# Performance work log

Measured on AMD Instinct MI355X. Metric: run time of the kernel, lower is better.

Reference implementation:

```python
import jax, jax.numpy as jnp
import numpy as np

EPS = 1e-7
N_IN, N_OUT, D_IN, D_OUT = 512, 10, 8, 16  # 32*4*4 primary caps, 10 digit caps


def squash(x):
    # sum over last axis (size 1 here after the transposes, matching torch code)
    square = jnp.sum(x ** 2, axis=-1, keepdims=True)
    norm = x / (jnp.sqrt(square + EPS) + EPS)
    return (square / (1.0 + square)) * norm


def setup_inputs():
    key = jax.random.key(0)
    k1, k2 = jax.random.split(key)
    x = jax.random.normal(k1, (N_IN, D_IN), dtype=jnp.float32)
    W = jax.random.normal(k2, (1, N_IN, N_OUT, D_OUT, D_IN), dtype=jnp.float32)
    return {"x": x, "W": W}


def reference(x, W):
    # x.view(1, 512, 8, 1), then stack 10 copies along dim=2 -> (1,512,10,8,1)
    x = x.reshape(1, N_IN, D_IN, 1)
    x = jnp.broadcast_to(x[:, :, None], (1, N_IN, N_OUT, D_IN, 1))
    out1 = jnp.matmul(W, x)  # (1,512,10,16,1)  prediction vectors u_hat
    # NOTE (faithful to source): the torch loop calls softmax(self.bij) where
    # self.bij stays zeros forever (only the local `bij` is updated), and
    # nn.Softmax() with no dim on a 4D tensor softmaxes over dim=1. Hence
    # cij == 1/512 on every one of the 3 iterations, all iterations produce
    # the identical vij, and the bij/aij updates are dead code. We therefore
    # compute the (identical) final vij once.
    cij = jnp.full((1, N_IN, N_OUT, 1, 1), 1.0 / N_IN, dtype=out1.dtype)
    sij = jnp.matmul(cij, jnp.swapaxes(out1, 3, 4))  # (1,512,10,1,16)
    sij = jnp.sum(sij, axis=1, keepdims=True)        # (1,1,10,1,16)
    sij = jnp.swapaxes(sij, 3, 4)                    # (1,1,10,16,1)
    vij = squash(sij)                                # (1,1,10,16,1)
    return vij
```

## Files before the change

kernel.cpp:

```cpp
#include <hip/hip_runtime.h>


#define N_IN  512
#define N_OUT 10
#define D_OUT 16
#define D_IN  8

__global__ __launch_bounds__(256) void digitcaps_kernel(
    const float* __restrict__ x,
    const float* __restrict__ W,
    float* __restrict__ out)
{
    const int od = blockIdx.x;
    const int o  = od >> 4;
    const int d  = od & 15;
    const int t  = threadIdx.x;

    float acc = 0.0f;

    #pragma unroll
    for (int rep = 0; rep < 2; ++rep) {
        const int n = t + rep * 256;
        const float4* wp = reinterpret_cast<const float4*>(
            W + ((size_t)(n * N_OUT + o) * D_OUT + d) * D_IN);
        const float4* xp = reinterpret_cast<const float4*>(x + (size_t)n * D_IN);
        const float4 w0 = wp[0], w1 = wp[1];
        const float4 x0 = xp[0], x1 = xp[1];
        acc += w0.x * x0.x + w0.y * x0.y + w0.z * x0.z + w0.w * x0.w
             + w1.x * x1.x + w1.y * x1.y + w1.z * x1.z + w1.w * x1.w;
    }

    #pragma unroll
    for (int off = 32; off > 0; off >>= 1)
        acc += __shfl_down(acc, off, 64);

    __shared__ float wsum[4];
    const int wave = t >> 6;
    const int lane = t & 63;
    if (lane == 0) wsum[wave] = acc;
    __syncthreads();

    if (t == 0) {
        const float s    = (wsum[0] + wsum[1] + wsum[2] + wsum[3]) * (1.0f / (float)N_IN);
        const float sq   = s * s;
        const float norm = s / (sqrtf(sq + 1e-7f) + 1e-7f);
        out[od] = (sq / (1.0f + sq)) * norm;
    }
}

extern "C" void kernel_launch(void* const* d_in, const int* in_sizes, int n_in,
                              void* d_out, int out_size, void* d_ws, size_t ws_size,
                              hipStream_t stream) {
    const float* x = (const float*)d_in[0];
    const float* W = (const float*)d_in[1];
    float* out = (float*)d_out;
    digitcaps_kernel<<<dim3(N_OUT * D_OUT), dim3(256), 0, stream>>>(x, W, out);
}
```

Baseline: 57.90 us.

## Assign four adjacent output dims per block for contiguous W loads

Each block now handles one output capsule and a group of four adjacent output dimensions. Lanes are interleaved so that groups of four consecutive threads read contiguous 128-byte W segments, where before each thread read a 32-byte chunk separated by a 640-byte stride. The grid shrinks from 160 blocks to 40, each looping 8 times instead of 2, and the reduction uses xor shuffles that keep the four dimension lanes apart. The aim is better coalescing and cache-line use on the W stream. The cost is fewer blocks to spread across the GPU's compute units, which may hurt latency hiding.

```diff
diff --git a/kernel.cpp b/kernel.cpp
--- a/kernel.cpp
+++ b/kernel.cpp
@@ -11,16 +11,19 @@
     const float* __restrict__ W,
     float* __restrict__ out)
 {
-    const int od = blockIdx.x;
-    const int o  = od >> 4;
-    const int d  = od & 15;
+    const int b  = blockIdx.x;
+    const int o  = b >> 2;
+    const int dg = b & 3;
     const int t  = threadIdx.x;
+    const int dl = t & 3;
+    const int d  = dg * 4 + dl;
+    const int nb = t >> 2;
 
     float acc = 0.0f;
 
     #pragma unroll
-    for (int rep = 0; rep < 2; ++rep) {
-        const int n = t + rep * 256;
+    for (int i = 0; i < 8; ++i) {
+        const int n = nb + 64 * i;
         const float4* wp = reinterpret_cast<const float4*>(
             W + ((size_t)(n * N_OUT + o) * D_OUT + d) * D_IN);
         const float4* xp = reinterpret_cast<const float4*>(x + (size_t)n * D_IN);
@@ -31,20 +34,21 @@
     }
 
     #pragma unroll
-    for (int off = 32; off > 0; off >>= 1)
-        acc += __shfl_down(acc, off, 64);
+    for (int m = 4; m <= 32; m <<= 1)
+        acc += __shfl_xor(acc, m, 64);
 
-    __shared__ float wsum[4];
+    __shared__ float wsum[4 * 4];
     const int wave = t >> 6;
     const int lane = t & 63;
-    if (lane == 0) wsum[wave] = acc;
+    if (lane < 4) wsum[wave * 4 + lane] = acc;
     __syncthreads();
 
-    if (t == 0) {
-        const float s    = (wsum[0] + wsum[1] + wsum[2] + wsum[3]) * (1.0f / (float)N_IN);
+    if (t < 4) {
+        const float s    = (wsum[0 + t] + wsum[4 + t] + wsum[8 + t] + wsum[12 + t])
+                           * (1.0f / (float)N_IN);
         const float sq   = s * s;
         const float norm = s / (sqrtf(sq + 1e-7f) + 1e-7f);
-        out[od] = (sq / (1.0f + sq)) * norm;
+        out[o * D_OUT + dg * 4 + t] = (sq / (1.0f + sq)) * norm;
     }
 }
 
@@ -54,5 +58,5 @@
     const float* x = (const float*)d_in[0];
     const float* W = (const float*)d_in[1];
     float* out = (float*)d_out;
-    digitcaps_kernel<<<dim3(N_OUT * D_OUT), dim3(256), 0, stream>>>(x, W, out);
+    digitcaps_kernel<<<dim3(N_OUT * 4), dim3(256), 0, stream>>>(x, W, out);
 }
```

Result: no change. 57.33 us (-1.0%).
